# Kernel tuning notes

Measured on AMD Instinct MI355X. Metric: run time of the kernel, lower is better.

Reference implementation:

```python
import jax, jax.numpy as jnp
import numpy as np

N_FEATURES = 256
HIDDEN_DIM = 256
NUM_HEADS = 8
HEAD_DIM = HIDDEN_DIM // NUM_HEADS
SCALE = HEAD_DIM ** -0.5
H = W = 64


def setup_inputs() -> dict:
    key = jax.random.key(0)
    k1, k2, kq, kk, kv, kp, kb = jax.random.split(key, 7)
    s = 1.0 / np.sqrt(N_FEATURES)
    return {
        "x1": jax.random.normal(k1, (1, N_FEATURES, H, W), dtype=jnp.float32),
        "x2": jax.random.normal(k2, (1, N_FEATURES, H, W), dtype=jnp.float32),
        # 1x1 conv weights reduce to [out_ch, in_ch] matrices
        "Wq": jax.random.uniform(kq, (HIDDEN_DIM, N_FEATURES), jnp.float32, -s, s),
        "Wk": jax.random.uniform(kk, (HIDDEN_DIM, N_FEATURES), jnp.float32, -s, s),
        "Wv": jax.random.uniform(kv, (HIDDEN_DIM, N_FEATURES), jnp.float32, -s, s),
        "Wp": jax.random.uniform(kp, (N_FEATURES, HIDDEN_DIM), jnp.float32, -s, s),
        "bp": jax.random.uniform(kb, (N_FEATURES,), jnp.float32, -s, s),
    }


def reference(x1, x2, Wq, Wk, Wv, Wp, bp):
    B, C, Hh, Ww = x1.shape
    N = Hh * Ww
    # 1x1 convs == channel matmuls; reshape to [B, heads, head_dim, N]
    q = jnp.einsum('oc,bchw->bohw', Wq, x1).reshape(B, NUM_HEADS, HEAD_DIM, N)
    k = jnp.einsum('oc,bchw->bohw', Wk, x2).reshape(B, NUM_HEADS, HEAD_DIM, N)
    v = jnp.einsum('oc,bchw->bohw', Wv, x2).reshape(B, NUM_HEADS, HEAD_DIM, N)
    attn = jnp.einsum('bhcn,bhcm->bhnm', q, k) * SCALE
    attn = jax.nn.softmax(attn, axis=-1)
    fused = jnp.einsum('bhnm,bhcm->bhcn', attn, v)
    fused = fused.reshape(B, HIDDEN_DIM, Hh, Ww)  # requires hidden_dim == C
    out = jnp.einsum('oc,bchw->bohw', Wp, fused) + bp[None, :, None, None]
    return out
```

## Files before the change

kernel.cpp:

```cpp
#include <hip/hip_runtime.h>

#define NPOS 4096
#define NCH  256
#define HD   32
#define KB   64

#define TOFF(o, c) (((((o) >> 4) * 8 + ((c) >> 5)) * 64 + \
                     ((((c) >> 3) & 3) * 16) + ((o) & 15)) * 8 + ((c) & 7))

typedef float f32x4  __attribute__((ext_vector_type(4)));
typedef float f32x16 __attribute__((ext_vector_type(16)));
typedef short s16x8  __attribute__((ext_vector_type(8)));
typedef uint  u32x2  __attribute__((ext_vector_type(2)));
typedef uint  u32x4  __attribute__((ext_vector_type(4)));
typedef int   i32x2  __attribute__((ext_vector_type(2)));

static __device__ __forceinline__ s16x8 load8(const ushort* p) {
    return *(const s16x8*)p;
}
static __device__ __forceinline__ ushort bfbits(float x) {
    __bf16 b = (__bf16)x;
    return __builtin_bit_cast(unsigned short, b);
}
static __device__ __forceinline__ float bfval(ushort u) {
    uint x = (uint)u << 16;
    return __builtin_bit_cast(float, x);
}
static __device__ __forceinline__ uint pk2(float a, float b) {
    return (uint)bfbits(a) | ((uint)bfbits(b) << 16);
}
static __device__ __forceinline__ void plswap(uint& a, uint& b) {
    i32x2 r = __builtin_amdgcn_permlane32_swap((int)a, (int)b, false, false);
    a = (uint)r[0];
    b = (uint)r[1];
}

__global__ __launch_bounds__(256) void convert_w_kernel(
    const float* __restrict__ Wq, const float* __restrict__ Wk,
    const float* __restrict__ Wv, const float* __restrict__ Wp,
    ushort* __restrict__ wsp, float qscale)
{
    const int m = blockIdx.y;
    const float* src = m == 0 ? Wq : m == 1 ? Wk : m == 2 ? Wv : Wp;
    const float sc = m == 0 ? qscale : 1.f;
    const int idx = (blockIdx.x * 256 + threadIdx.x) * 4;
    const int o = idx >> 8, c0 = idx & 255;
    f32x4 w = *(const f32x4*)(src + idx);
    w *= sc;
    ushort h[4], l[4];
#pragma unroll
    for (int i = 0; i < 4; ++i) {
        h[i] = bfbits(w[i]);
        l[i] = bfbits(w[i] - bfval(h[i]));
    }
    ushort* H = wsp + m * 2 * 65536;
    const int off = TOFF(o, c0);
    *(u32x2*)(H + off)         = (u32x2){(uint)h[0] | ((uint)h[1] << 16),
                                         (uint)h[2] | ((uint)h[3] << 16)};
    *(u32x2*)(H + 65536 + off) = (u32x2){(uint)l[0] | ((uint)l[1] << 16),
                                         (uint)l[2] | ((uint)l[3] << 16)};
}

__global__ __launch_bounds__(256) void fused_qkv_kernel(
    const float* __restrict__ x1, const float* __restrict__ x2,
    const ushort* __restrict__ wsp,
    ushort* __restrict__ qt, ushort* __restrict__ kt, ushort* __restrict__ vt)
{
    __shared__ __align__(16) ushort lds[32768];
    const int tid   = threadIdx.x;
    const int n0    = blockIdx.x * 32;
    const int obase = blockIdx.y * 128;

    {
        const int ln = tid & 7;
        const int cr = tid >> 3;
#pragma unroll
        for (int pass = 0; pass < 16; ++pass) {
            const int c = (pass & 7) * 32 + cr;
            const float* X = (pass < 8) ? x1 : x2;
            const int rbase = (pass < 8) ? 0 : 16384;
            const f32x4 v = *(const f32x4*)(X + (size_t)c * NPOS + n0 + ln * 4);
#pragma unroll
            for (int i = 0; i < 4; ++i) {
                const int nl = ln * 4 + i;
                const ushort hb = bfbits(v[i]);
                const ushort lb = bfbits(v[i] - bfval(hb));
                const int idx = (((nl >> 4) * 8 + (c >> 5)) * 64 +
                                 (((c >> 3) & 3) * 16) + (nl & 15)) * 8 + (c & 7);
                lds[rbase + idx]        = hb;
                lds[rbase + 8192 + idx] = lb;
            }
        }
    }
    __syncthreads();

    const int wid = tid >> 6, lane = tid & 63;
    const int lq = lane & 15, grp = lane >> 4;

    f32x4 acc[3][2][2];
#pragma unroll
    for (int m = 0; m < 3; ++m)
#pragma unroll
        for (int ot = 0; ot < 2; ++ot)
#pragma unroll
            for (int nt = 0; nt < 2; ++nt)
                acc[m][ot][nt] = (f32x4){0.f, 0.f, 0.f, 0.f};

#pragma unroll
    for (int kc = 0; kc < 8; ++kc) {
#pragma unroll
        for (int m = 0; m < 3; ++m) {
            const ushort* W = wsp + m * 131072;
            const int bb = (m == 0) ? 0 : 16384;
#pragma unroll
            for (int ot = 0; ot < 2; ++ot) {
                const int To = (obase + (wid * 2 + ot) * 16) >> 4;
                const s16x8 ah = load8(W + ((To * 8 + kc) * 64 + lane) * 8);
                const s16x8 al = load8(W + 65536 + ((To * 8 + kc) * 64 + lane) * 8);
#pragma unroll
                for (int nt = 0; nt < 2; ++nt) {
                    const s16x8 bh = *(const s16x8*)(lds + bb +
                                        ((nt * 8 + kc) * 64 + lane) * 8);
                    const s16x8 bl = *(const s16x8*)(lds + bb + 8192 +
                                        ((nt * 8 + kc) * 64 + lane) * 8);
                    acc[m][ot][nt] = __builtin_amdgcn_mfma_f32_16x16x32_bf16(
                        ah, bh, acc[m][ot][nt], 0, 0, 0);
                    acc[m][ot][nt] = __builtin_amdgcn_mfma_f32_16x16x32_bf16(
                        ah, bl, acc[m][ot][nt], 0, 0, 0);
                    acc[m][ot][nt] = __builtin_amdgcn_mfma_f32_16x16x32_bf16(
                        al, bh, acc[m][ot][nt], 0, 0, 0);
                }
            }
        }
    }

#pragma unroll
    for (int m = 0; m < 3; ++m)
#pragma unroll
        for (int ot = 0; ot < 2; ++ot) {
            const int o0 = obase + (wid * 2 + ot) * 16;
            if (m < 2) {
                ushort* Y = m ? kt : qt;
                const int head = o0 >> 5, d0 = (o0 & 31) + grp * 4;
#pragma unroll
                for (int nt = 0; nt < 2; ++nt) {
                    const int n = n0 + nt * 16 + lq;
                    *(u32x2*)(Y + head * (NPOS * HD) + n * HD + d0) =
                        (u32x2){pk2(acc[m][ot][nt][0], acc[m][ot][nt][1]),
                                pk2(acc[m][ot][nt][2], acc[m][ot][nt][3])};
                }
            } else {
#pragma unroll
                for (int nt = 0; nt < 2; ++nt) {
                    const int n = n0 + nt * 16 + lq;
#pragma unroll
                    for (int r = 0; r < 4; ++r)
                        vt[(o0 + grp * 4 + r) * NPOS + n] =
                            bfbits(acc[2][ot][nt][r]);
                }
            }
        }
}

template <int NS>
__global__ __launch_bounds__(256) void attn_mfma_kernel(
    const ushort* __restrict__ Qt,
    const ushort* __restrict__ Kt,
    const ushort* __restrict__ Vt,
    ushort* __restrict__ Opb,
    float* __restrict__ Ml)
{
    constexpr int SPLIT = NPOS / NS;
    constexpr int NSTEP = SPLIT / KB;
    __shared__ __align__(16) ushort lds[9728];
    const int bid  = blockIdx.x;
    const int s    = bid >> 8;
    const int h    = bid & 7;
    const int qblk = (bid & 255) >> 3;
    const int tid  = threadIdx.x;
    const int wid  = tid >> 6;
    const int lane = tid & 63;
    const int l31  = lane & 31;
    const int hi   = lane >> 5;
    const int q0   = qblk * 128 + wid * 32;
    const int k0   = s * SPLIT;
    const int hq   = h * (NPOS * HD);

    s16x8 qf[2];
#pragma unroll
    for (int kh = 0; kh < 2; ++kh)
        qf[kh] = load8(Qt + hq + (q0 + l31) * HD + kh * 16 + hi * 8);

    const int kr0 = tid >> 2, kc0 = tid & 3;
    const ushort* kS = Kt + hq + kr0 * HD + kc0 * 8;
    const int kdst = kr0 * 40 + (((kc0 ^ (kr0 >> 3)) & 3) << 3);

    const int vr0 = tid >> 3, vc0 = tid & 7;
    const ushort* vS = Vt + h * (HD * NPOS) + vr0 * NPOS + vc0 * 8;
    const int vdst = vr0 * 72 + (((vc0 ^ (vr0 >> 3)) & 7) << 3);

    const int kx = l31 >> 3;

    f32x16 oacc = {};
    float lacc = 0.f;

    *(s16x8*)(lds + kdst)        = load8(kS + (size_t)k0 * HD);
    *(s16x8*)(lds + 5120 + vdst) = load8(vS + k0);
    const int m1 = (NSTEP > 1) ? k0 + KB : k0;
    s16x8 kra = load8(kS + (size_t)m1 * HD);
    s16x8 vra = load8(vS + m1);
    __syncthreads();

    for (int step = 0; step < NSTEP; ++step) {
        const int cur = step & 1;
        ushort* const Kb = lds + cur * 2560;
        ushort* const Vb = lds + 5120 + cur * 2304;

        {
            ushort* const Kn = lds + (cur ^ 1) * 2560;
            ushort* const Vn = lds + 5120 + (cur ^ 1) * 2304;
            *(s16x8*)(Kn + kdst) = kra;
            *(s16x8*)(Vn + vdst) = vra;
        }
        const int mn = (step + 2 < NSTEP) ? k0 + (step + 2) * KB : k0;
        kra = load8(kS + (size_t)mn * HD);
        vra = load8(vS + mn);

#pragma unroll
        for (int t = 0; t < 2; ++t) {
            const int krow = (t * 32 + l31) * 40;
            const s16x8 kfa = *(const s16x8*)(Kb + krow + (((hi ^ kx) & 3) << 3));
            const s16x8 kfb = *(const s16x8*)(Kb + krow + ((((2 + hi) ^ kx) & 3) << 3));
            f32x16 st = {};
            __builtin_amdgcn_s_setprio(1);
            st = __builtin_amdgcn_mfma_f32_32x32x16_bf16(kfa, qf[0], st, 0, 0, 0);
            st = __builtin_amdgcn_mfma_f32_32x32x16_bf16(kfb, qf[1], st, 0, 0, 0);
            __builtin_amdgcn_s_setprio(0);

            const s16x8 vf0 = *(const s16x8*)(Vb + l31 * 72 +
                                              ((((t * 4 + hi) ^ kx) & 7) << 3));
            const s16x8 vf1 = *(const s16x8*)(Vb + l31 * 72 +
                                              ((((t * 4 + 2 + hi) ^ kx) & 7) << 3));

            uint w[4], w2[4];
            float ls = 0.f;
#pragma unroll
            for (int g = 0; g < 4; ++g) {
                const float p0 = __builtin_amdgcn_exp2f(st[4 * g + 0]);
                const float p1 = __builtin_amdgcn_exp2f(st[4 * g + 1]);
                const float p2 = __builtin_amdgcn_exp2f(st[4 * g + 2]);
                const float p3 = __builtin_amdgcn_exp2f(st[4 * g + 3]);
                ls += (p0 + p1) + (p2 + p3);
                w[g]  = pk2(p0, p1);
                w2[g] = pk2(p2, p3);
            }
            lacc += ls;
            uint a0 = w[0],  c0 = w[1];  plswap(a0, c0);
            uint a1 = w2[0], c1 = w2[1]; plswap(a1, c1);
            const s16x8 pfA = __builtin_bit_cast(s16x8, (u32x4){a0, a1, c0, c1});
            uint b0 = w[2],  d0 = w[3];  plswap(b0, d0);
            uint b1 = w2[2], d1 = w2[3]; plswap(b1, d1);
            const s16x8 pfB = __builtin_bit_cast(s16x8, (u32x4){b0, b1, d0, d1});

            __builtin_amdgcn_s_setprio(1);
            oacc = __builtin_amdgcn_mfma_f32_32x32x16_bf16(vf0, pfA, oacc, 0, 0, 0);
            oacc = __builtin_amdgcn_mfma_f32_32x32x16_bf16(vf1, pfB, oacc, 0, 0, 0);
            __builtin_amdgcn_s_setprio(0);
        }

        __syncthreads();
    }

    {
        uint a = __builtin_bit_cast(uint, lacc), b = a;
        plswap(a, b);
        lacc = __builtin_bit_cast(float, a) + __builtin_bit_cast(float, b);
    }

    const int n = q0 + l31;
    ushort* Ops = Opb + (size_t)s * (NPOS * NCH) + n * NCH + h * HD;
#pragma unroll
    for (int g = 0; g < 4; ++g) {
        *(u32x2*)(Ops + g * 8 + hi * 4) =
            (u32x2){pk2(oacc[4 * g + 0], oacc[4 * g + 1]),
                    pk2(oacc[4 * g + 2], oacc[4 * g + 3])};
    }
    if (lane < 32)
        Ml[(s * 8 + h) * NPOS + n] = lacc;
}

template <int NS>
__global__ __launch_bounds__(256) void fused_out_kernel(
    const ushort* __restrict__ Opb, const float* __restrict__ Ml,
    const ushort* __restrict__ Wh, const ushort* __restrict__ Wl,
    const float* __restrict__ bias, float* __restrict__ Y)
{
    __shared__ __align__(16) ushort lds[8192];
    const int tid = threadIdx.x;
    const int n0  = blockIdx.x * 16;

    {
        const int nl = tid >> 4;
        const int c0 = (tid & 15) * 16;
        const int n  = n0 + nl;
        const int h  = c0 >> 5;
        float l = 0.f;
#pragma unroll
        for (int s = 0; s < NS; ++s)
            l += Ml[(s * 8 + h) * NPOS + n];
        const float inv = 1.f / l;

        float f[16];
#pragma unroll
        for (int i = 0; i < 16; ++i) f[i] = 0.f;
#pragma unroll
        for (int s = 0; s < NS; ++s) {
            const s16x8 r0 = load8(Opb + (size_t)s * (NPOS * NCH) + n * NCH + c0);
            const s16x8 r1 = load8(Opb + (size_t)s * (NPOS * NCH) + n * NCH + c0 + 8);
#pragma unroll
            for (int i = 0; i < 8; ++i) {
                f[i]     += bfval((ushort)r0[i]);
                f[i + 8] += bfval((ushort)r1[i]);
            }
        }
#pragma unroll
        for (int i = 0; i < 16; ++i) {
            const int c = c0 + i;
            const float v = f[i] * inv;
            const ushort hb = bfbits(v);
            const ushort lb = bfbits(v - bfval(hb));
            const int idx = ((c >> 5) * 64 + (((c >> 3) & 3) * 16) + nl) * 8 + (c & 7);
            lds[idx]        = hb;
            lds[4096 + idx] = lb;
        }
    }
    __syncthreads();

    const int wid = tid >> 6, lane = tid & 63;
    const int lq = lane & 15, grp = lane >> 4;

    f32x4 acc[4];
#pragma unroll
    for (int ot = 0; ot < 4; ++ot) acc[ot] = (f32x4){0.f, 0.f, 0.f, 0.f};

#pragma unroll
    for (int kc = 0; kc < 8; ++kc) {
        const s16x8 bh = *(const s16x8*)(lds + (kc * 64 + lane) * 8);
        const s16x8 bl = *(const s16x8*)(lds + 4096 + (kc * 64 + lane) * 8);
#pragma unroll
        for (int ot = 0; ot < 4; ++ot) {
            const int To = wid * 4 + ot;
            const s16x8 ah = load8(Wh + ((To * 8 + kc) * 64 + lane) * 8);
            const s16x8 al = load8(Wl + ((To * 8 + kc) * 64 + lane) * 8);
            acc[ot] = __builtin_amdgcn_mfma_f32_16x16x32_bf16(ah, bh, acc[ot], 0, 0, 0);
            acc[ot] = __builtin_amdgcn_mfma_f32_16x16x32_bf16(ah, bl, acc[ot], 0, 0, 0);
            acc[ot] = __builtin_amdgcn_mfma_f32_16x16x32_bf16(al, bh, acc[ot], 0, 0, 0);
        }
    }

#pragma unroll
    for (int ot = 0; ot < 4; ++ot) {
        const int o0 = (wid * 4 + ot) * 16;
        const f32x4 b4 = *(const f32x4*)(bias + o0 + grp * 4);
#pragma unroll
        for (int r = 0; r < 4; ++r)
            Y[(o0 + grp * 4 + r) * NPOS + n0 + lq] = acc[ot][r] + b4[r];
    }
}

extern "C" void kernel_launch(void* const* d_in, const int* in_sizes, int n_in,
                              void* d_out, int out_size, void* d_ws, size_t ws_size,
                              hipStream_t stream) {
    const float* x1 = (const float*)d_in[0];
    const float* x2 = (const float*)d_in[1];
    const float* Wq = (const float*)d_in[2];
    const float* Wk = (const float*)d_in[3];
    const float* Wv = (const float*)d_in[4];
    const float* Wp = (const float*)d_in[5];
    const float* bp = (const float*)d_in[6];
    float* out = (float*)d_out;

    const size_t MB = 1u << 20;
    char* wsc = (char*)d_ws;
    const float qscale = (float)(0.17677669529663687 * 1.4426950408889634);

    if (ws_size >= 25 * MB) {
        ushort* Opb = (ushort*)(wsc + 0 * MB);
        ushort* qt  = (ushort*)(wsc + 16 * MB);
        ushort* kt  = (ushort*)(wsc + 18 * MB);
        ushort* vt  = (ushort*)(wsc + 20 * MB);
        ushort* wsp = (ushort*)(wsc + 22 * MB);
        float*  Ml  = (float*)(wsc + 23 * MB + 256 * 1024);

        convert_w_kernel<<<dim3(64, 4), 256, 0, stream>>>(
            Wq, Wk, Wv, Wp, wsp, qscale);
        fused_qkv_kernel<<<dim3(128, 2), 256, 0, stream>>>(
            x1, x2, wsp, qt, kt, vt);
        attn_mfma_kernel<8><<<2048, 256, 0, stream>>>(qt, kt, vt, Opb, Ml);
        fused_out_kernel<8><<<256, 256, 0, stream>>>(
            Opb, Ml, wsp + 393216, wsp + 458752, bp, out);
    } else {
        ushort* Opb = (ushort*)(wsc + 0 * MB);
        ushort* qt  = (ushort*)(wsc + 8 * MB);
        ushort* kt  = (ushort*)(wsc + 10 * MB);
        ushort* vt  = (ushort*)(wsc + 12 * MB);
        ushort* wsp = (ushort*)(wsc + 14 * MB);
        float*  Ml  = (float*)(wsc + 15 * MB);

        convert_w_kernel<<<dim3(64, 4), 256, 0, stream>>>(
            Wq, Wk, Wv, Wp, wsp, qscale);
        fused_qkv_kernel<<<dim3(128, 2), 256, 0, stream>>>(
            x1, x2, wsp, qt, kt, vt);
        attn_mfma_kernel<4><<<1024, 256, 0, stream>>>(qt, kt, vt, Opb, Ml);
        fused_out_kernel<4><<<256, 256, 0, stream>>>(
            Opb, Ml, wsp + 393216, wsp + 458752, bp, out);
    }
}
```

Measured before the change: 76.93 us.

## Process two query tiles per wave to reuse K/V fragments in attention

Each wave now handles 64 query rows (two 32-row tiles) instead of 32, so every K and V fragment read from shared memory feeds two sets of MFMAs. The grid shrinks by half and the block index mapping changes so that query blocks vary fastest. This cuts LDS traffic and global K/V staging per query, in exchange for more registers (two accumulators plus extra Q fragments) and fewer blocks, which may lower occupancy and parallelism.

```diff
diff --git a/kernel.cpp b/kernel.cpp
--- a/kernel.cpp
+++ b/kernel.cpp
@@ -174,22 +174,24 @@
     constexpr int NSTEP = SPLIT / KB;
     __shared__ __align__(16) ushort lds[9728];
     const int bid  = blockIdx.x;
-    const int s    = bid >> 8;
-    const int h    = bid & 7;
-    const int qblk = (bid & 255) >> 3;
+    const int s    = bid >> 7;
+    const int h    = (bid >> 4) & 7;
+    const int qblk = bid & 15;
     const int tid  = threadIdx.x;
     const int wid  = tid >> 6;
     const int lane = tid & 63;
     const int l31  = lane & 31;
     const int hi   = lane >> 5;
-    const int q0   = qblk * 128 + wid * 32;
+    const int q0   = qblk * 256 + wid * 64;
     const int k0   = s * SPLIT;
     const int hq   = h * (NPOS * HD);
 
-    s16x8 qf[2];
-#pragma unroll
-    for (int kh = 0; kh < 2; ++kh)
-        qf[kh] = load8(Qt + hq + (q0 + l31) * HD + kh * 16 + hi * 8);
+    s16x8 qf[2][2];
+#pragma unroll
+    for (int qt = 0; qt < 2; ++qt)
+#pragma unroll
+        for (int kh = 0; kh < 2; ++kh)
+            qf[qt][kh] = load8(Qt + hq + (q0 + qt * 32 + l31) * HD + kh * 16 + hi * 8);
 
     const int kr0 = tid >> 2, kc0 = tid & 3;
     const ushort* kS = Kt + hq + kr0 * HD + kc0 * 8;
@@ -201,8 +203,8 @@
 
     const int kx = l31 >> 3;
 
-    f32x16 oacc = {};
-    float lacc = 0.f;
+    f32x16 oaccA = {}, oaccB = {};
+    float laccA = 0.f, laccB = 0.f;
 
     *(s16x8*)(lds + kdst)        = load8(kS + (size_t)k0 * HD);
     *(s16x8*)(lds + 5120 + vdst) = load8(vS + k0);
@@ -231,62 +233,77 @@
             const int krow = (t * 32 + l31) * 40;
             const s16x8 kfa = *(const s16x8*)(Kb + krow + (((hi ^ kx) & 3) << 3));
             const s16x8 kfb = *(const s16x8*)(Kb + krow + ((((2 + hi) ^ kx) & 3) << 3));
-            f32x16 st = {};
-            __builtin_amdgcn_s_setprio(1);
-            st = __builtin_amdgcn_mfma_f32_32x32x16_bf16(kfa, qf[0], st, 0, 0, 0);
-            st = __builtin_amdgcn_mfma_f32_32x32x16_bf16(kfb, qf[1], st, 0, 0, 0);
-            __builtin_amdgcn_s_setprio(0);
-
             const s16x8 vf0 = *(const s16x8*)(Vb + l31 * 72 +
                                               ((((t * 4 + hi) ^ kx) & 7) << 3));
             const s16x8 vf1 = *(const s16x8*)(Vb + l31 * 72 +
                                               ((((t * 4 + 2 + hi) ^ kx) & 7) << 3));
 
-            uint w[4], w2[4];
-            float ls = 0.f;
-#pragma unroll
-            for (int g = 0; g < 4; ++g) {
-                const float p0 = __builtin_amdgcn_exp2f(st[4 * g + 0]);
-                const float p1 = __builtin_amdgcn_exp2f(st[4 * g + 1]);
-                const float p2 = __builtin_amdgcn_exp2f(st[4 * g + 2]);
-                const float p3 = __builtin_amdgcn_exp2f(st[4 * g + 3]);
-                ls += (p0 + p1) + (p2 + p3);
-                w[g]  = pk2(p0, p1);
-                w2[g] = pk2(p2, p3);
+#pragma unroll
+            for (int qt = 0; qt < 2; ++qt) {
+                f32x16 st = {};
+                __builtin_amdgcn_s_setprio(1);
+                st = __builtin_amdgcn_mfma_f32_32x32x16_bf16(
+                    kfa, qf[qt][0], st, 0, 0, 0);
+                st = __builtin_amdgcn_mfma_f32_32x32x16_bf16(
+                    kfb, qf[qt][1], st, 0, 0, 0);
+                __builtin_amdgcn_s_setprio(0);
+
+                uint w[4], w2[4];
+                float ls = 0.f;
+#pragma unroll
+                for (int g = 0; g < 4; ++g) {
+                    const float p0 = __builtin_amdgcn_exp2f(st[4 * g + 0]);
+                    const float p1 = __builtin_amdgcn_exp2f(st[4 * g + 1]);
+                    const float p2 = __builtin_amdgcn_exp2f(st[4 * g + 2]);
+                    const float p3 = __builtin_amdgcn_exp2f(st[4 * g + 3]);
+                    ls += (p0 + p1) + (p2 + p3);
+                    w[g]  = pk2(p0, p1);
+                    w2[g] = pk2(p2, p3);
+                }
+                uint a0 = w[0],  c0 = w[1];  plswap(a0, c0);
+                uint a1 = w2[0], c1 = w2[1]; plswap(a1, c1);
+                const s16x8 pfA = __builtin_bit_cast(s16x8, (u32x4){a0, a1, c0, c1});
+                uint b0 = w[2],  d0 = w[3];  plswap(b0, d0);
+                uint b1 = w2[2], d1 = w2[3]; plswap(b1, d1);
+                const s16x8 pfB = __builtin_bit_cast(s16x8, (u32x4){b0, b1, d0, d1});
+
+                __builtin_amdgcn_s_setprio(1);
+                if (qt == 0) {
+                    laccA += ls;
+                    oaccA = __builtin_amdgcn_mfma_f32_32x32x16_bf16(vf0, pfA, oaccA, 0, 0, 0);
+                    oaccA = __builtin_amdgcn_mfma_f32_32x32x16_bf16(vf1, pfB, oaccA, 0, 0, 0);
+                } else {
+                    laccB += ls;
+                    oaccB = __builtin_amdgcn_mfma_f32_32x32x16_bf16(vf0, pfA, oaccB, 0, 0, 0);
+                    oaccB = __builtin_amdgcn_mfma_f32_32x32x16_bf16(vf1, pfB, oaccB, 0, 0, 0);
+                }
+                __builtin_amdgcn_s_setprio(0);
             }
-            lacc += ls;
-            uint a0 = w[0],  c0 = w[1];  plswap(a0, c0);
-            uint a1 = w2[0], c1 = w2[1]; plswap(a1, c1);
-            const s16x8 pfA = __builtin_bit_cast(s16x8, (u32x4){a0, a1, c0, c1});
-            uint b0 = w[2],  d0 = w[3];  plswap(b0, d0);
-            uint b1 = w2[2], d1 = w2[3]; plswap(b1, d1);
-            const s16x8 pfB = __builtin_bit_cast(s16x8, (u32x4){b0, b1, d0, d1});
-
-            __builtin_amdgcn_s_setprio(1);
-            oacc = __builtin_amdgcn_mfma_f32_32x32x16_bf16(vf0, pfA, oacc, 0, 0, 0);
-            oacc = __builtin_amdgcn_mfma_f32_32x32x16_bf16(vf1, pfB, oacc, 0, 0, 0);
-            __builtin_amdgcn_s_setprio(0);
         }
 
         __syncthreads();
     }
 
-    {
-        uint a = __builtin_bit_cast(uint, lacc), b = a;
-        plswap(a, b);
-        lacc = __builtin_bit_cast(float, a) + __builtin_bit_cast(float, b);
-    }
-
-    const int n = q0 + l31;
-    ushort* Ops = Opb + (size_t)s * (NPOS * NCH) + n * NCH + h * HD;
-#pragma unroll
-    for (int g = 0; g < 4; ++g) {
-        *(u32x2*)(Ops + g * 8 + hi * 4) =
-            (u32x2){pk2(oacc[4 * g + 0], oacc[4 * g + 1]),
-                    pk2(oacc[4 * g + 2], oacc[4 * g + 3])};
-    }
-    if (lane < 32)
-        Ml[(s * 8 + h) * NPOS + n] = lacc;
+#pragma unroll
+    for (int qt = 0; qt < 2; ++qt) {
+        float lacc = qt ? laccB : laccA;
+        {
+            uint a = __builtin_bit_cast(uint, lacc), b = a;
+            plswap(a, b);
+            lacc = __builtin_bit_cast(float, a) + __builtin_bit_cast(float, b);
+        }
+        const f32x16& oacc = qt ? oaccB : oaccA;
+        const int n = q0 + qt * 32 + l31;
+        ushort* Ops = Opb + (size_t)s * (NPOS * NCH) + n * NCH + h * HD;
+#pragma unroll
+        for (int g = 0; g < 4; ++g) {
+            *(u32x2*)(Ops + g * 8 + hi * 4) =
+                (u32x2){pk2(oacc[4 * g + 0], oacc[4 * g + 1]),
+                        pk2(oacc[4 * g + 2], oacc[4 * g + 3])};
+        }
+        if (lane < 32)
+            Ml[(s * 8 + h) * NPOS + n] = lacc;
+    }
 }
 
 template <int NS>
@@ -396,7 +413,7 @@
             Wq, Wk, Wv, Wp, wsp, qscale);
         fused_qkv_kernel<<<dim3(128, 2), 256, 0, stream>>>(
             x1, x2, wsp, qt, kt, vt);
-        attn_mfma_kernel<8><<<2048, 256, 0, stream>>>(qt, kt, vt, Opb, Ml);
+        attn_mfma_kernel<8><<<1024, 256, 0, stream>>>(qt, kt, vt, Opb, Ml);
         fused_out_kernel<8><<<256, 256, 0, stream>>>(
             Opb, Ml, wsp + 393216, wsp + 458752, bp, out);
     } else {
@@ -411,7 +428,7 @@
             Wq, Wk, Wv, Wp, wsp, qscale);
         fused_qkv_kernel<<<dim3(128, 2), 256, 0, stream>>>(
             x1, x2, wsp, qt, kt, vt);
-        attn_mfma_kernel<4><<<1024, 256, 0, stream>>>(qt, kt, vt, Opb, Ml);
+        attn_mfma_kernel<4><<<512, 256, 0, stream>>>(qt, kt, vt, Opb, Ml);
         fused_out_kernel<4><<<256, 256, 0, stream>>>(
             Opb, Ml, wsp + 393216, wsp + 458752, bp, out);
     }
```

After: 76.63 us. About the same (-0.4%).
